# Kernel optimization log

Hardware: AMD Instinct MI355X
Metric: run time of the kernel (lower is better)

Reference implementation:

```python
import jax, jax.numpy as jnp
import numpy as np

N = 2048
NONGT = 2048
EMB = 64
GROUP = 16
FEAT = 256
DM = 1024  # dim[0] == dim[1]
DHEAD = DM // GROUP  # 64


def setup_inputs() -> dict:
    key = jax.random.key(0)
    ks = jax.random.split(key, 12)
    s = lambda fan_in: 1.0 / np.sqrt(fan_in)
    return {
        "roi_feat": jax.random.normal(ks[0], (N, FEAT), jnp.float32),
        "position_embedding": jax.random.uniform(ks[1], (N, NONGT, EMB), jnp.float32),
        "fc1_w": jax.random.normal(ks[2], (GROUP, EMB), jnp.float32) * s(EMB),
        "fc1_b": jnp.zeros((GROUP,), jnp.float32),
        "fc2_w": jax.random.normal(ks[3], (DM, FEAT), jnp.float32) * s(FEAT),
        "fc2_b": jnp.zeros((DM,), jnp.float32),
        "fc3_w": jax.random.normal(ks[4], (DM, FEAT), jnp.float32) * s(FEAT),
        "fc3_b": jnp.zeros((DM,), jnp.float32),
        "conv_w": jax.random.normal(ks[5], (FEAT, GROUP * FEAT), jnp.float32) * s(GROUP * FEAT),
        "conv_b": jnp.zeros((FEAT,), jnp.float32),
        "nongt_dim": NONGT,
    }


def reference(roi_feat, position_embedding, fc1_w, fc1_b, fc2_w, fc2_b,
              fc3_w, fc3_b, conv_w, conv_b, nongt_dim):
    nongt_roi_feat = roi_feat[:nongt_dim, :]                      # [M, FEAT]
    # position bias: relu(fc1(pe)) -> [N, M, G] -> [N, G, M]
    pos1 = jax.nn.relu(jnp.einsum('nme,ge->nmg', position_embedding, fc1_w) + fc1_b)
    aff_weight = jnp.transpose(pos1, (0, 2, 1))                   # [N, G, M]
    # grouped Q, K
    q = roi_feat @ fc2_w.T + fc2_b                                # [N, DM]
    q = q.reshape(-1, GROUP, DHEAD)                               # [N, G, d]
    k = nongt_roi_feat @ fc3_w.T + fc3_b                          # [M, DM]
    k = k.reshape(-1, GROUP, DHEAD)                               # [M, G, d]
    scale = 1.0 / np.sqrt(float(DHEAD))
    aff = jnp.einsum('ngd,mgd->ngm', q, k) * scale                # [N, G, M]
    weighted = jnp.log(jnp.maximum(aff_weight, 1e-6)) + aff
    aff_softmax = jax.nn.softmax(weighted, axis=-1)               # [N, G, M]
    out_t = jnp.einsum('ngm,mc->ngc', aff_softmax, nongt_roi_feat)  # [N, G, FEAT]
    flat = out_t.reshape(out_t.shape[0], GROUP * FEAT)            # channel order g*FEAT + c
    return flat @ conv_w.T + conv_b                               # [N, FEAT]
```

## Files before the change

### kernel.cpp

```cpp
#include <hip/hip_runtime.h>
#include <hip/hip_bf16.h>

#define NQ   2048
#define NK   2048
#define EMB  64
#define GRP  16
#define FEAT 256

typedef __bf16 bf16x8 __attribute__((ext_vector_type(8)));
typedef __bf16 bf16x4 __attribute__((ext_vector_type(4)));
typedef float  f32x4  __attribute__((ext_vector_type(4)));

#define MFMA(a, b, c) __builtin_amdgcn_mfma_f32_16x16x32_bf16((a), (b), (c), 0, 0, 0)

typedef __attribute__((address_space(3))) unsigned int  lds_u32;
typedef __attribute__((address_space(1))) unsigned int  glb_u32;

static __device__ __forceinline__ bf16x8 cvt8(float4 a, float4 b) {
    bf16x8 r;
    r[0] = (__bf16)a.x; r[1] = (__bf16)a.y; r[2] = (__bf16)a.z; r[3] = (__bf16)a.w;
    r[4] = (__bf16)b.x; r[5] = (__bf16)b.y; r[6] = (__bf16)b.z; r[7] = (__bf16)b.w;
    return r;
}

__launch_bounds__(256, 2)
__global__ void prep_all(const float* __restrict__ roi,
                         const float* __restrict__ pe,
                         const float* __restrict__ fc1w,
                         const float* __restrict__ fc1b,
                         const float* __restrict__ fc2w,
                         const float* __restrict__ fc2b,
                         const float* __restrict__ fc3w,
                         const float* __restrict__ fc3b,
                         const float* __restrict__ cw,
                         __bf16* __restrict__ roiT,
                         __bf16* __restrict__ convwb,
                         __bf16* __restrict__ qb,
                         __bf16* __restrict__ kb,
                         __bf16* __restrict__ wg) {
    __shared__ float tile[64][65];
    const int b   = blockIdx.x;
    const int tid = threadIdx.x;

    if (b < 128) {
        const int m0 = (b >> 2) * 64, c0 = (b & 3) * 64;
        const int tr = tid >> 4, tc = tid & 15;
#pragma unroll
        for (int ch = 0; ch < 4; ++ch) {
            int r = ch * 16 + tr;
            float4 v = *(const float4*)(roi + (m0 + r) * 256 + c0 + tc * 4);
            tile[r][tc * 4 + 0] = v.x; tile[r][tc * 4 + 1] = v.y;
            tile[r][tc * 4 + 2] = v.z; tile[r][tc * 4 + 3] = v.w;
        }
        __syncthreads();
#pragma unroll
        for (int ch = 0; ch < 4; ++ch) {
            int crow = ch * 16 + tr;
            int mm = tc * 4;
            bf16x4 o;
            o[0] = (__bf16)tile[mm + 0][crow]; o[1] = (__bf16)tile[mm + 1][crow];
            o[2] = (__bf16)tile[mm + 2][crow]; o[3] = (__bf16)tile[mm + 3][crow];
            *(bf16x4*)(roiT + (c0 + crow) * 2048 + m0 + mm) = o;
        }
    } else if (b < 640) {
        const int cb = b - 128;
        for (int i = cb * 256 + tid; i < 262144; i += 512 * 256) {
            float4 v = ((const float4*)cw)[i];
            bf16x4 o;
            o[0] = (__bf16)v.x; o[1] = (__bf16)v.y; o[2] = (__bf16)v.z; o[3] = (__bf16)v.w;
            ((bf16x4*)convwb)[i] = o;
        }
    } else if (b < 1664) {
        const int qi = b - 640;
        const int x  = qi & 511;
        const int isK = qi >> 9;
        const float* W    = isK ? fc3w : fc2w;
        const float* bias = isK ? fc3b : fc2b;
        __bf16*      out  = isK ? kb   : qb;
        const int l = tid & 63, wid = tid >> 6;
        const int n0 = (x >> 2) * 16;
        const int dmB = (x & 3) * 256 + wid * 64;
        const int lr = l & 15, lk = l >> 4;
        f32x4 acc[4];
#pragma unroll
        for (int i = 0; i < 4; ++i) acc[i] = (f32x4){0.f, 0.f, 0.f, 0.f};
        for (int k0 = 0; k0 < 256; k0 += 32) {
            const float* ap = roi + (n0 + lr) * 256 + k0 + lk * 8;
            bf16x8 af = cvt8(*(const float4*)ap, *(const float4*)(ap + 4));
#pragma unroll
            for (int cf = 0; cf < 4; ++cf) {
                const float* bp = W + (dmB + cf * 16 + lr) * 256 + k0 + lk * 8;
                acc[cf] = MFMA(af, cvt8(*(const float4*)bp, *(const float4*)(bp + 4)), acc[cf]);
            }
        }
#pragma unroll
        for (int cf = 0; cf < 4; ++cf) {
            int dm = dmB + cf * 16 + lr;
            float bv = bias[dm];
            int g = dm >> 6, d = dm & 63;
#pragma unroll
            for (int ri = 0; ri < 4; ++ri) {
                int n = n0 + lk * 4 + ri;
                out[(g * 2048 + n) * 64 + d] = (__bf16)(acc[cf][ri] + bv);
            }
        }
    } else {
        const int wb = b - 1664;
        const int l = tid & 63, wid = tid >> 6;
        const int lr = l & 15, lk = l >> 4;
        const long n = wb >> 2;
        const int mbase = (wb & 3) * 512 + wid * 128;

        bf16x8 fcB[2];
#pragma unroll
        for (int s = 0; s < 2; ++s) {
            const float* p = fc1w + lr * 64 + s * 32 + lk * 8;
            fcB[s] = cvt8(*(const float4*)p, *(const float4*)(p + 4));
        }
        const float bias = fc1b[lr];

        const float* pebase = pe + (n * 2048 + mbase + lr) * 64 + lk * 8;
        __bf16* obase = wg + (n * 16 + lr) * 2048 + mbase + lk * 4;

#pragma unroll 4
        for (int it = 0; it < 8; ++it) {
            const float* p0 = pebase + it * 16 * 64;
            f32x4 c = (f32x4){0.f, 0.f, 0.f, 0.f};
            c = MFMA(cvt8(*(const float4*)(p0),      *(const float4*)(p0 + 4)),  fcB[0], c);
            c = MFMA(cvt8(*(const float4*)(p0 + 32), *(const float4*)(p0 + 36)), fcB[1], c);
            bf16x4 o;
#pragma unroll
            for (int ri = 0; ri < 4; ++ri)
                o[ri] = (__bf16)fmaxf(fmaxf(c[ri] + bias, 0.f), 1e-6f);
            *(bf16x4*)(obase + it * 16) = o;
        }
    }
}

#define P_BASE 65536
__launch_bounds__(256, 2)
__global__ void relation_attn(const __bf16* __restrict__ wg,
                              const __bf16* __restrict__ qb,
                              const __bf16* __restrict__ kb,
                              const __bf16* __restrict__ roiT,
                              __bf16* __restrict__ flat) {
    __shared__ __align__(16) unsigned char smem[81920];
    const int tid = threadIdx.x;
    const int l   = tid & 63;
    const int wid = tid >> 6;
    const int s_  = ((blockIdx.x & 7) << 6) | (blockIdx.x >> 3);
    const int n0  = (s_ & 255) * 8;
    const int ghalf = s_ >> 8;
    const int lr  = l & 15;
    const int lk  = l >> 4;
    const int gh  = lk >> 1;
    const int nqh = lk & 1;
    const int g2  = ghalf * 8 + wid * 2;
    const int gA  = g2 + gh;

    bf16x8 qa[2][2];
#pragma unroll
    for (int gi = 0; gi < 2; ++gi)
#pragma unroll
        for (int s = 0; s < 2; ++s)
            qa[gi][s] = *(const bf16x8*)(qb + (long)((g2 + gi) * 2048 + n0 + (lr & 7)) * 64 + s * 32 + lk * 8);

    f32x4 acc[16];
#pragma unroll
    for (int i = 0; i < 16; ++i) acc[i] = (f32x4){0.f, 0.f, 0.f, 0.f};
    float dsum[4] = {0.f, 0.f, 0.f, 0.f};

    const __bf16* wptr = wg + (long)((n0 + (nqh << 2)) * 16 + gA) * 2048 + lr;

    for (int t = 0; t < 16; ++t) {
        const int m0t = t * 128;
        __syncthreads();

        {
            const int crow = l >> 3, slot = l & 7;
#pragma unroll
            for (int i = 0; i < 16; ++i) {
                int row  = wid * 64 + (i & 7) * 8 + crow;
                int D    = ((i >> 3) << 3) | (slot ^ (row & 7));
                const __bf16* gp = roiT + row * 2048 + m0t + D * 8;
                __builtin_amdgcn_global_load_lds(
                    (const glb_u32*)(const void*)gp,
                    (lds_u32*)(void*)(smem + wid * 16384 + i * 1024), 16, 0, 0);
            }
        }

#pragma unroll
        for (int h = 0; h < 2; ++h) {
            const int mb = m0t + h * 64;

            float wlv[4][4];
#pragma unroll
            for (int mf = 0; mf < 4; ++mf)
#pragma unroll
                for (int ri = 0; ri < 4; ++ri)
                    wlv[mf][ri] = (float)wptr[(long)ri * 32768 + mb + mf * 16];

            __builtin_amdgcn_s_setprio(1);
            f32x4 a0[4], a1[4];
#pragma unroll
            for (int mf = 0; mf < 4; ++mf) {
                const __bf16* kp = kb + (long)(g2 * 2048 + mb + mf * 16 + lr) * 64 + lk * 8;
                bf16x8 k0 = *(const bf16x8*)(kp);
                bf16x8 k1 = *(const bf16x8*)(kp + 32);
                f32x4 z = (f32x4){0.f, 0.f, 0.f, 0.f};
                z = MFMA(qa[0][0], k0, z);
                z = MFMA(qa[0][1], k1, z);
                a0[mf] = z;
            }
#pragma unroll
            for (int mf = 0; mf < 4; ++mf) {
                const __bf16* kp = kb + (long)((g2 + 1) * 2048 + mb + mf * 16 + lr) * 64 + lk * 8;
                bf16x8 k0 = *(const bf16x8*)(kp);
                bf16x8 k1 = *(const bf16x8*)(kp + 32);
                f32x4 z = (f32x4){0.f, 0.f, 0.f, 0.f};
                z = MFMA(qa[1][0], k0, z);
                z = MFMA(qa[1][1], k1, z);
                a1[mf] = z;
            }
            __builtin_amdgcn_s_setprio(0);

#pragma unroll
            for (int mf = 0; mf < 4; ++mf) {
                int mm = h * 64 + mf * 16 + lr;
#pragma unroll
                for (int ri = 0; ri < 4; ++ri) {
                    float a = gh ? a1[mf][ri] : a0[mf][ri];
                    int n2 = (nqh << 2) + ri;
                    float pv = wlv[mf][ri] * __expf(a * 0.125f);
                    dsum[ri] += pv;
                    int rp = ((gA & 7) << 3) + n2;
                    int poff = (rp << 8) + ((mm ^ (n2 << 3)) << 1);
                    *(__bf16*)(smem + P_BASE + poff) = (__bf16)pv;
                }
            }
        }

        __syncthreads();

        {
            const int rpA = wid * 16 + lr;
            const int QA = (rpA & 7) << 3;
            __builtin_amdgcn_s_setprio(1);
#pragma unroll
            for (int s = 0; s < 4; ++s) {
                bf16x8 pA = *(const bf16x8*)(smem + P_BASE + (rpA << 8)
                                             + (((s * 32 + lk * 8) ^ QA) << 1));
                const int c4 = s * 4 + lk;
#pragma unroll
                for (int cf = 0; cf < 16; ++cf) {
                    int r = cf * 16 + lr;
                    bf16x8 rB = *(const bf16x8*)(smem
                        + (((r >> 6) * 2 + (c4 >> 3)) << 13)
                        + ((r & 63) << 7)
                        + ((((c4 & 7) ^ (r & 7))) << 4));
                    acc[cf] = MFMA(pA, rB, acc[cf]);
                }
            }
            __builtin_amdgcn_s_setprio(0);
        }
    }

    float inv[4];
#pragma unroll
    for (int ri = 0; ri < 4; ++ri) {
        float v = dsum[ri];
        v += __shfl_xor(v, 1); v += __shfl_xor(v, 2);
        v += __shfl_xor(v, 4); v += __shfl_xor(v, 8);
        inv[ri] = 1.0f / v;
    }
#pragma unroll
    for (int cf = 0; cf < 16; ++cf) {
        int c = cf * 16 + lr;
#pragma unroll
        for (int ri = 0; ri < 4; ++ri) {
            int n2 = (nqh << 2) + ri;
            flat[(long)(n0 + n2) * 4096 + gA * 256 + c] = (__bf16)(acc[cf][ri] * inv[ri]);
        }
    }
}

__launch_bounds__(256)
__global__ void conv_gemm(const __bf16* __restrict__ flat, const __bf16* __restrict__ cw,
                          const float* __restrict__ cb, float* __restrict__ out) {
    const int tid = threadIdx.x, l = tid & 63, wid = tid >> 6;
    const int n0 = (blockIdx.x >> 1) * 16;
    const int j0 = (blockIdx.x & 1) * 128 + wid * 32;
    const int lr = l & 15, lk = l >> 4;
    f32x4 acc[2] = {(f32x4){0.f, 0.f, 0.f, 0.f}, (f32x4){0.f, 0.f, 0.f, 0.f}};
#pragma unroll 4
    for (int k0 = 0; k0 < 4096; k0 += 32) {
        bf16x8 af = *(const bf16x8*)(flat + (long)(n0 + lr) * 4096 + k0 + lk * 8);
#pragma unroll
        for (int cf = 0; cf < 2; ++cf) {
            bf16x8 bfr = *(const bf16x8*)(cw + (long)(j0 + cf * 16 + lr) * 4096 + k0 + lk * 8);
            acc[cf] = MFMA(af, bfr, acc[cf]);
        }
    }
#pragma unroll
    for (int cf = 0; cf < 2; ++cf) {
        int j = j0 + cf * 16 + lr;
        float bv = cb[j];
#pragma unroll
        for (int ri = 0; ri < 4; ++ri)
            out[(n0 + lk * 4 + ri) * 256 + j] = acc[cf][ri] + bv;
    }
}

extern "C" void kernel_launch(void* const* d_in, const int* in_sizes, int n_in,
                              void* d_out, int out_size, void* d_ws, size_t ws_size,
                              hipStream_t stream) {
    const float* roi  = (const float*)d_in[0];
    const float* pe   = (const float*)d_in[1];
    const float* fc1w = (const float*)d_in[2];
    const float* fc1b = (const float*)d_in[3];
    const float* fc2w = (const float*)d_in[4];
    const float* fc2b = (const float*)d_in[5];
    const float* fc3w = (const float*)d_in[6];
    const float* fc3b = (const float*)d_in[7];
    const float* cw   = (const float*)d_in[8];
    const float* cb   = (const float*)d_in[9];
    float* out = (float*)d_out;

    unsigned char* ws = (unsigned char*)d_ws;
    __bf16* roiT   = (__bf16*)(ws);
    __bf16* convwb = (__bf16*)(ws + (1ull  << 20));
    __bf16* qb     = (__bf16*)(ws + (3ull  << 20));
    __bf16* kb     = (__bf16*)(ws + (7ull  << 20));
    __bf16* flat   = (__bf16*)(ws + (11ull << 20));
    __bf16* wg     = (__bf16*)(ws + (27ull << 20));

    prep_all<<<9856, 256, 0, stream>>>(roi, pe, fc1w, fc1b, fc2w, fc2b,
                                       fc3w, fc3b, cw,
                                       roiT, convwb, qb, kb, wg);
    relation_attn<<<512, 256, 0, stream>>>(wg, qb, kb, roiT, flat);
    conv_gemm<<<256, 256, 0, stream>>>(flat, convwb, cb, out);
}
```

Baseline: 487.8 us.

## Fuse position-bias computation into attention kernel with inter-block flag handshake

Moves the fc1+relu position-weight computation out of the prep kernel and into relation_attn, where each block pair computes its share of the wg tile one step ahead and exchanges readiness through global atomic flags. The intent is to overlap the 1 GB fp32 position-embedding stream with attention compute and drop a separate large kernel pass. It adds a per-tile spin-wait between paired blocks, which can deadlock if the partner block is not co-resident and adds synchronisation stalls. It also keeps writing wg to global memory rather than removing that round trip.

```diff
diff --git a/kernel.cpp b/kernel.cpp
--- a/kernel.cpp
+++ b/kernel.cpp
@@ -24,20 +24,17 @@
 }
 
 __launch_bounds__(256, 2)
-__global__ void prep_all(const float* __restrict__ roi,
-                         const float* __restrict__ pe,
-                         const float* __restrict__ fc1w,
-                         const float* __restrict__ fc1b,
-                         const float* __restrict__ fc2w,
-                         const float* __restrict__ fc2b,
-                         const float* __restrict__ fc3w,
-                         const float* __restrict__ fc3b,
-                         const float* __restrict__ cw,
-                         __bf16* __restrict__ roiT,
-                         __bf16* __restrict__ convwb,
-                         __bf16* __restrict__ qb,
-                         __bf16* __restrict__ kb,
-                         __bf16* __restrict__ wg) {
+__global__ void prep_small(const float* __restrict__ roi,
+                           const float* __restrict__ fc2w,
+                           const float* __restrict__ fc2b,
+                           const float* __restrict__ fc3w,
+                           const float* __restrict__ fc3b,
+                           const float* __restrict__ cw,
+                           __bf16* __restrict__ roiT,
+                           __bf16* __restrict__ convwb,
+                           __bf16* __restrict__ qb,
+                           __bf16* __restrict__ kb,
+                           int* __restrict__ flags) {
     __shared__ float tile[64][65];
     const int b   = blockIdx.x;
     const int tid = threadIdx.x;
@@ -105,52 +102,29 @@
             }
         }
     } else {
-        const int wb = b - 1664;
-        const int l = tid & 63, wid = tid >> 6;
-        const int lr = l & 15, lk = l >> 4;
-        const long n = wb >> 2;
-        const int mbase = (wb & 3) * 512 + wid * 128;
-
-        bf16x8 fcB[2];
-#pragma unroll
-        for (int s = 0; s < 2; ++s) {
-            const float* p = fc1w + lr * 64 + s * 32 + lk * 8;
-            fcB[s] = cvt8(*(const float4*)p, *(const float4*)(p + 4));
-        }
-        const float bias = fc1b[lr];
-
-        const float* pebase = pe + (n * 2048 + mbase + lr) * 64 + lk * 8;
-        __bf16* obase = wg + (n * 16 + lr) * 2048 + mbase + lk * 4;
-
-#pragma unroll 4
-        for (int it = 0; it < 8; ++it) {
-            const float* p0 = pebase + it * 16 * 64;
-            f32x4 c = (f32x4){0.f, 0.f, 0.f, 0.f};
-            c = MFMA(cvt8(*(const float4*)(p0),      *(const float4*)(p0 + 4)),  fcB[0], c);
-            c = MFMA(cvt8(*(const float4*)(p0 + 32), *(const float4*)(p0 + 36)), fcB[1], c);
-            bf16x4 o;
-#pragma unroll
-            for (int ri = 0; ri < 4; ++ri)
-                o[ri] = (__bf16)fmaxf(fmaxf(c[ri] + bias, 0.f), 1e-6f);
-            *(bf16x4*)(obase + it * 16) = o;
-        }
+        for (int i = tid; i < 8192; i += 256) flags[i] = 0;
     }
 }
 
 #define P_BASE 65536
 __launch_bounds__(256, 2)
-__global__ void relation_attn(const __bf16* __restrict__ wg,
+__global__ void relation_attn(const float* __restrict__ pe,
+                              const float* __restrict__ fc1w,
+                              const float* __restrict__ fc1b,
                               const __bf16* __restrict__ qb,
                               const __bf16* __restrict__ kb,
                               const __bf16* __restrict__ roiT,
+                              __bf16* __restrict__ wg,
+                              int* __restrict__ flags,
                               __bf16* __restrict__ flat) {
     __shared__ __align__(16) unsigned char smem[81920];
     const int tid = threadIdx.x;
     const int l   = tid & 63;
     const int wid = tid >> 6;
-    const int s_  = ((blockIdx.x & 7) << 6) | (blockIdx.x >> 3);
-    const int n0  = (s_ & 255) * 8;
-    const int ghalf = s_ >> 8;
+    const int bid = blockIdx.x;
+    const int ghalf = (bid >> 3) & 1;
+    const int chunk = ((bid >> 4) << 3) | (bid & 7);
+    const int n0  = chunk * 8;
     const int lr  = l & 15;
     const int lk  = l >> 4;
     const int gh  = lk >> 1;
@@ -165,16 +139,53 @@
         for (int s = 0; s < 2; ++s)
             qa[gi][s] = *(const bf16x8*)(qb + (long)((g2 + gi) * 2048 + n0 + (lr & 7)) * 64 + s * 32 + lk * 8);
 
+    bf16x8 fcB[2];
+#pragma unroll
+    for (int s = 0; s < 2; ++s) {
+        const float* p = fc1w + lr * 64 + s * 32 + lk * 8;
+        fcB[s] = cvt8(*(const float4*)p, *(const float4*)(p + 4));
+    }
+    const float wbias = fc1b[lr];
+
     f32x4 acc[16];
 #pragma unroll
     for (int i = 0; i < 16; ++i) acc[i] = (f32x4){0.f, 0.f, 0.f, 0.f};
     float dsum[4] = {0.f, 0.f, 0.f, 0.f};
 
     const __bf16* wptr = wg + (long)((n0 + (nqh << 2)) * 16 + gA) * 2048 + lr;
+    int* flg = flags + chunk * 32;
+
+    {
+        const int mb = ghalf * 64;
+#pragma unroll
+        for (int j = 0; j < 2; ++j) {
+            const long nq = n0 + wid * 2 + j;
+            const float* pb = pe + (nq * 2048 + mb + lr) * 64 + lk * 8;
+            __bf16* ob = wg + (nq * 16 + lr) * 2048 + mb + lk * 4;
+#pragma unroll
+            for (int mf = 0; mf < 4; ++mf) {
+                const float* pr = pb + mf * 16 * 64;
+                f32x4 c = (f32x4){0.f, 0.f, 0.f, 0.f};
+                c = MFMA(cvt8(*(const float4*)(pr),      *(const float4*)(pr + 4)),  fcB[0], c);
+                c = MFMA(cvt8(*(const float4*)(pr + 32), *(const float4*)(pr + 36)), fcB[1], c);
+                bf16x4 o;
+#pragma unroll
+                for (int ri = 0; ri < 4; ++ri)
+                    o[ri] = (__bf16)fmaxf(fmaxf(c[ri] + wbias, 0.f), 1e-6f);
+                *(bf16x4*)(ob + mf * 16) = o;
+            }
+        }
+    }
 
     for (int t = 0; t < 16; ++t) {
         const int m0t = t * 128;
         __syncthreads();
+
+        if (tid == 0) {
+            __threadfence();
+            __hip_atomic_store(flg + t * 2 + ghalf, 1,
+                               __ATOMIC_RELEASE, __HIP_MEMORY_SCOPE_AGENT);
+        }
 
         {
             const int crow = l >> 3, slot = l & 7;
@@ -188,6 +199,35 @@
                     (lds_u32*)(void*)(smem + wid * 16384 + i * 1024), 16, 0, 0);
             }
         }
+
+        if (t < 15) {
+            const int mb = (t + 1) * 128 + ghalf * 64;
+#pragma unroll
+            for (int j = 0; j < 2; ++j) {
+                const long nq = n0 + wid * 2 + j;
+                const float* pb = pe + (nq * 2048 + mb + lr) * 64 + lk * 8;
+                __bf16* ob = wg + (nq * 16 + lr) * 2048 + mb + lk * 4;
+#pragma unroll
+                for (int mf = 0; mf < 4; ++mf) {
+                    const float* pr = pb + mf * 16 * 64;
+                    f32x4 c = (f32x4){0.f, 0.f, 0.f, 0.f};
+                    c = MFMA(cvt8(*(const float4*)(pr),      *(const float4*)(pr + 4)),  fcB[0], c);
+                    c = MFMA(cvt8(*(const float4*)(pr + 32), *(const float4*)(pr + 36)), fcB[1], c);
+                    bf16x4 o;
+#pragma unroll
+                    for (int ri = 0; ri < 4; ++ri)
+                        o[ri] = (__bf16)fmaxf(fmaxf(c[ri] + wbias, 0.f), 1e-6f);
+                    *(bf16x4*)(ob + mf * 16) = o;
+                }
+            }
+        }
+
+        if (tid == 0) {
+            while (__hip_atomic_load(flg + t * 2 + (ghalf ^ 1),
+                                     __ATOMIC_ACQUIRE, __HIP_MEMORY_SCOPE_AGENT) == 0)
+                __builtin_amdgcn_s_sleep(8);
+        }
+        __syncthreads();
 
 #pragma unroll
         for (int h = 0; h < 2; ++h) {
@@ -333,10 +373,11 @@
     __bf16* kb     = (__bf16*)(ws + (7ull  << 20));
     __bf16* flat   = (__bf16*)(ws + (11ull << 20));
     __bf16* wg     = (__bf16*)(ws + (27ull << 20));
-
-    prep_all<<<9856, 256, 0, stream>>>(roi, pe, fc1w, fc1b, fc2w, fc2b,
-                                       fc3w, fc3b, cw,
-                                       roiT, convwb, qb, kb, wg);
-    relation_attn<<<512, 256, 0, stream>>>(wg, qb, kb, roiT, flat);
+    int*    flags  = (int*)  (ws + (156ull << 20));
+
+    prep_small<<<1665, 256, 0, stream>>>(roi, fc2w, fc2b, fc3w, fc3b, cw,
+                                         roiT, convwb, qb, kb, flags);
+    relation_attn<<<512, 256, 0, stream>>>(pe, fc1w, fc1b, qb, kb, roiT,
+                                           wg, flags, flat);
     conv_gemm<<<256, 256, 0, stream>>>(flat, convwb, cb, out);
 }
```

Result: slower. 1.232 ms (+152.6%).
